# Optimization experiments

Hardware: AMD Instinct MI355X
Metric: run time of the kernel (lower is better)

## Reference

```python
import jax, jax.numpy as jnp
import numpy as np

DIM = 1024
HEADS = 16
HEAD_DIM = DIM // HEADS
EPS = 1e-5


def layer_norm(x, w, b):
    # normalize over last dim (head_dim)
    mu = jnp.mean(x, axis=-1, keepdims=True)
    var = jnp.mean(jnp.square(x - mu), axis=-1, keepdims=True)
    return (x - mu) * jax.lax.rsqrt(var + EPS) * w + b


def setup_inputs() -> dict:
    key = jax.random.key(0)
    ks = jax.random.split(key, 8)
    B, N = 2, 2048
    x = jax.random.normal(ks[0], (B, N, DIM), dtype=jnp.float32)
    mask = jax.random.randint(ks[1], (B, 1, N, N), 0, 2) == 1  # True = masked out
    qkv_w = jax.random.normal(ks[2], (3 * DIM, DIM), dtype=jnp.float32) * (DIM ** -0.5)
    q_norm_w = jnp.ones((HEAD_DIM,), dtype=jnp.float32)
    q_norm_b = jnp.zeros((HEAD_DIM,), dtype=jnp.float32)
    k_norm_w = jnp.ones((HEAD_DIM,), dtype=jnp.float32)
    k_norm_b = jnp.zeros((HEAD_DIM,), dtype=jnp.float32)
    proj_w = jax.random.normal(ks[3], (DIM, DIM), dtype=jnp.float32) * (DIM ** -0.5)
    proj_b = jnp.zeros((DIM,), dtype=jnp.float32)
    return {"x": x, "mask": mask, "qkv_w": qkv_w,
            "q_norm_w": q_norm_w, "q_norm_b": q_norm_b,
            "k_norm_w": k_norm_w, "k_norm_b": k_norm_b,
            "proj_w": proj_w, "proj_b": proj_b}


def reference(x, mask, qkv_w, q_norm_w, q_norm_b, k_norm_w, k_norm_b, proj_w, proj_b):
    B, N, C = x.shape
    H, D = HEADS, HEAD_DIM
    scale = D ** -0.5
    # qkv projection (no bias), split into q,k,v of shape (B,H,N,D)
    qkv = (x @ qkv_w.T).reshape(B, N, 3, H, D).transpose(2, 0, 3, 1, 4)
    q, k, v = qkv[0], qkv[1], qkv[2]
    q = layer_norm(q, q_norm_w, q_norm_b)
    k = layer_norm(k, k_norm_w, k_norm_b)
    q = q * scale
    attn = jnp.einsum("bhnd,bhmd->bhnm", q, k)  # (B,H,N,N)
    attn = jnp.where(mask, -jnp.inf, attn)
    attn = jax.nn.softmax(attn, axis=-1)
    out = jnp.einsum("bhnm,bhmd->bhnd", attn, v)
    out = out.transpose(0, 2, 1, 3).reshape(B, N, C)
    return out @ proj_w.T + proj_b
```

## Files before the change

kernel.cpp:

```cpp
#include <hip/hip_runtime.h>
#include <hip/hip_bf16.h>
#include <math.h>

#define B_    2
#define N_    2048
#define DIM_  1024
#define H_    16
#define HD_   64
#define EPS_  1e-5f
#define SCALE_ 0.125f
#define LOG2E_ 1.4426950408889634f
#define MFIX_  14.0f

typedef __attribute__((ext_vector_type(8))) __bf16 bf16x8;
typedef __attribute__((ext_vector_type(8))) unsigned short ushort8;
typedef __attribute__((ext_vector_type(4))) float f32x4;
typedef __attribute__((ext_vector_type(4))) unsigned int uint4v;

__device__ __forceinline__ unsigned short f2bf(float x) {
    unsigned u = __builtin_bit_cast(unsigned, x);
    u += 0x7fff + ((u >> 16) & 1);
    return (unsigned short)(u >> 16);
}
__device__ __forceinline__ unsigned pk2bf(float a, float b) {
    unsigned ua = __builtin_bit_cast(unsigned, a) + 0x8000u;
    unsigned ub = __builtin_bit_cast(unsigned, b) + 0x8000u;
    return __builtin_amdgcn_perm(ub, ua, 0x07060302);
}
__device__ __forceinline__ unsigned cvtpk(float a, float b) {
    unsigned r;
    asm("v_cvt_pk_bf16_f32 %0, %1, %2" : "=v"(r) : "v"(a), "v"(b));
    return r;
}

__device__ __forceinline__ void gl_lds16(const void* g, void* l) {
    __builtin_amdgcn_global_load_lds(
        (const __attribute__((address_space(1))) void*)g,
        (__attribute__((address_space(3))) void*)l, 16, 0, 0);
}

__global__ __launch_bounds__(256) void cast_all_bf16(
    const float* __restrict__ x, const float* __restrict__ qkvw,
    const float* __restrict__ pw, unsigned short* __restrict__ out) {
    int i = (blockIdx.x * 256 + threadIdx.x) * 8;
    const float* src;
    if (i < 4194304) src = x + i;
    else if (i < 7340032) src = qkvw + (i - 4194304);
    else src = pw + (i - 7340032);
    float4 v0 = *(const float4*)src;
    float4 v1 = *(const float4*)(src + 4);
    ushort8 r;
    r[0] = f2bf(v0.x); r[1] = f2bf(v0.y); r[2] = f2bf(v0.z); r[3] = f2bf(v0.w);
    r[4] = f2bf(v1.x); r[5] = f2bf(v1.y); r[6] = f2bf(v1.z); r[7] = f2bf(v1.w);
    *(ushort8*)(out + i) = r;
}

__global__ __launch_bounds__(256) void pack_mask(
    const int* __restrict__ mask, unsigned long long* __restrict__ bm) {
    int w = blockIdx.x * 4 + (threadIdx.x >> 6);
    int lane = threadIdx.x & 63;
    int mv = mask[(size_t)w * 64 + lane];
    unsigned long long bits = __ballot(mv != 0);
    if (lane == 0) bm[w] = bits;
}

__global__ __launch_bounds__(256) void gemm_qkv_ln(
    const unsigned short* __restrict__ A, const unsigned short* __restrict__ Bw,
    const float* __restrict__ qnw, const float* __restrict__ qnb,
    const float* __restrict__ knw, const float* __restrict__ knb,
    unsigned short* __restrict__ qbuf, unsigned short* __restrict__ kbuf,
    unsigned short* __restrict__ vt) {
    const int K = DIM_;
    __shared__ unsigned short As[128 * 32];
    __shared__ unsigned short Bs[128 * 32];
    const int tid = threadIdx.x;
    const int wave = tid >> 6, lane = tid & 63;
    const int quad = lane >> 4, lcol = lane & 15;
    const int wr = wave >> 1, wc = wave & 1;
    const int row0 = blockIdx.y * 128, col0 = blockIdx.x * 128;

    f32x4 acc[4][4];
#pragma unroll
    for (int i = 0; i < 4; ++i)
#pragma unroll
        for (int j = 0; j < 4; ++j) acc[i][j] = (f32x4){0.f, 0.f, 0.f, 0.f};

    for (int k0 = 0; k0 < K; k0 += 32) {
        __syncthreads();
#pragma unroll
        for (int c = 0; c < 2; ++c) {
            int base = wave * 2048 + c * 1024;
            int myofs = base + lane * 16;
            int r = myofs >> 6;
            int kb = myofs & 63;
            gl_lds16((const char*)A + ((size_t)(row0 + r) * K + k0) * 2 + kb,
                     (char*)As + base);
            gl_lds16((const char*)Bw + ((size_t)(col0 + r) * K + k0) * 2 + kb,
                     (char*)Bs + base);
        }
        __syncthreads();

        bf16x8 af[4], bfr[4];
#pragma unroll
        for (int i = 0; i < 4; ++i) {
            af[i] = *(const bf16x8*)&As[(wr * 64 + i * 16 + lcol) * 32 + quad * 8];
            bfr[i] = *(const bf16x8*)&Bs[(wc * 64 + i * 16 + lcol) * 32 + quad * 8];
        }
#pragma unroll
        for (int i = 0; i < 4; ++i)
#pragma unroll
            for (int j = 0; j < 4; ++j)
                acc[i][j] = __builtin_amdgcn_mfma_f32_16x16x32_bf16(
                    af[i], bfr[j], acc[i][j], 0, 0, 0);
    }

    const int colbase = col0 + wc * 64;
    const int t = colbase >> 10;
    const int h = (colbase & 1023) >> 6;

    if (t < 2) {
        const float* wv = (t == 0) ? qnw : knw;
        const float* bv = (t == 0) ? qnb : knb;
        float wreg[4], breg[4];
#pragma unroll
        for (int j = 0; j < 4; ++j) {
            wreg[j] = wv[j * 16 + lcol];
            breg[j] = bv[j * 16 + lcol];
        }
        const float sc = (t == 0) ? (SCALE_ * LOG2E_) : 1.f;
        unsigned short* obase = (t == 0) ? qbuf : kbuf;
#pragma unroll
        for (int i = 0; i < 4; ++i) {
#pragma unroll
            for (int reg = 0; reg < 4; ++reg) {
                int row = row0 + wr * 64 + i * 16 + quad * 4 + reg;
                int bb = row >> 11, n = row & (N_ - 1);
                float v[4];
#pragma unroll
                for (int j = 0; j < 4; ++j) v[j] = acc[i][j][reg];
                float s = v[0] + v[1] + v[2] + v[3];
                s += __shfl_xor(s, 1);
                s += __shfl_xor(s, 2);
                s += __shfl_xor(s, 4);
                s += __shfl_xor(s, 8);
                float mu = s * (1.f / 64.f);
                float d[4], s2 = 0.f;
#pragma unroll
                for (int j = 0; j < 4; ++j) {
                    d[j] = v[j] - mu;
                    s2 += d[j] * d[j];
                }
                s2 += __shfl_xor(s2, 1);
                s2 += __shfl_xor(s2, 2);
                s2 += __shfl_xor(s2, 4);
                s2 += __shfl_xor(s2, 8);
                float r = rsqrtf(s2 * (1.f / 64.f) + EPS_);
                float o0 = (d[0] * r * wreg[0] + breg[0]) * sc;
                float o1 = (d[1] * r * wreg[1] + breg[1]) * sc;
                float o2 = (d[2] * r * wreg[2] + breg[2]) * sc;
                float o3 = (d[3] * r * wreg[3] + breg[3]) * sc;
                uint2 pk;
                pk.x = pk2bf(o0, o1);
                pk.y = pk2bf(o2, o3);
                *(uint2*)(obase + ((size_t)(bb * H_ + h) * N_ + n) * 64 +
                          lcol * 4) = pk;
            }
        }
    } else {
        const int rowb = row0 + wr * 64;
        const int bb = rowb >> 11;
        unsigned short* vtb =
            vt + ((size_t)(bb * H_ + h) * 64) * (size_t)N_ + (rowb & (N_ - 1));
#pragma unroll
        for (int i = 0; i < 4; ++i) {
            const int pos = (i >> 1) * 32 + quad * 8 + (i & 1) * 4;
#pragma unroll
            for (int jj = 0; jj < 4; ++jj) {
                uint2 pk;
                pk.x = pk2bf(acc[i][jj][0], acc[i][jj][1]);
                pk.y = pk2bf(acc[i][jj][2], acc[i][jj][3]);
                *(uint2*)(vtb + (size_t)(lcol + 16 * jj) * N_ + pos) = pk;
            }
        }
    }
}

__global__ __launch_bounds__(256) void gemm_proj(
    const unsigned short* __restrict__ A, const unsigned short* __restrict__ Bw,
    const float* __restrict__ bias, float* __restrict__ Cout) {
    const int K = DIM_;
    __shared__ unsigned short As[128 * 32];
    __shared__ unsigned short Bs[64 * 32];
    const int tid = threadIdx.x;
    const int wave = tid >> 6, lane = tid & 63;
    const int quad = lane >> 4, lcol = lane & 15;
    const int row0 = blockIdx.y * 128, col0 = blockIdx.x * 64;

    f32x4 acc[2][4];
#pragma unroll
    for (int i = 0; i < 2; ++i)
#pragma unroll
        for (int j = 0; j < 4; ++j) acc[i][j] = (f32x4){0.f, 0.f, 0.f, 0.f};

    for (int k0 = 0; k0 < K; k0 += 32) {
        __syncthreads();
#pragma unroll
        for (int pi = 0; pi < 3; ++pi) {
            int p = wave * 3 + pi;
            if (p < 8) {
                int base = p * 1024;
                int myofs = base + lane * 16;
                int r = myofs >> 6, kb = myofs & 63;
                gl_lds16((const char*)A + ((size_t)(row0 + r) * K + k0) * 2 + kb,
                         (char*)As + base);
            } else {
                int base = (p - 8) * 1024;
                int myofs = base + lane * 16;
                int r = myofs >> 6, kb = myofs & 63;
                gl_lds16((const char*)Bw + ((size_t)(col0 + r) * K + k0) * 2 + kb,
                         (char*)Bs + base);
            }
        }
        __syncthreads();

        bf16x8 af[2], bfr[4];
#pragma unroll
        for (int i = 0; i < 2; ++i)
            af[i] = *(const bf16x8*)&As[(wave * 32 + i * 16 + lcol) * 32 + quad * 8];
#pragma unroll
        for (int j = 0; j < 4; ++j)
            bfr[j] = *(const bf16x8*)&Bs[(j * 16 + lcol) * 32 + quad * 8];
#pragma unroll
        for (int i = 0; i < 2; ++i)
#pragma unroll
            for (int j = 0; j < 4; ++j)
                acc[i][j] = __builtin_amdgcn_mfma_f32_16x16x32_bf16(
                    af[i], bfr[j], acc[i][j], 0, 0, 0);
    }

#pragma unroll
    for (int i = 0; i < 2; ++i) {
#pragma unroll
        for (int j = 0; j < 4; ++j) {
            int col = col0 + j * 16 + lcol;
            float bv = bias[col];
#pragma unroll
            for (int reg = 0; reg < 4; ++reg) {
                int row = row0 + wave * 32 + i * 16 + quad * 4 + reg;
                Cout[(size_t)row * DIM_ + col] = acc[i][j][reg] + bv;
            }
        }
    }
}

#define WB0                                                               \
    asm volatile("s_waitcnt vmcnt(0)" ::: "memory");                      \
    __builtin_amdgcn_s_barrier();                                         \
    __builtin_amdgcn_sched_barrier(0);

#define FISSUE(BUF, M0, M1)                                               \
    {                                                                     \
        gl_lds16(kp0, (char*)Ks[BUF] + kld0);                             \
        gl_lds16(kp1, (char*)Ks[BUF] + kld1);                             \
        gl_lds16(kp2, (char*)Ks[BUF] + kld2);                             \
        gl_lds16(kp3, (char*)Ks[BUF] + kld3);                             \
        gl_lds16(vp0, (char*)Vts[BUF] + kld0);                            \
        gl_lds16(vp1, (char*)Vts[BUF] + kld1);                            \
        gl_lds16(vp2, (char*)Vts[BUF] + kld2);                            \
        gl_lds16(vp3, (char*)Vts[BUF] + kld3);                            \
        M0 = *bmq0; M1 = *bmq1;                                           \
        kp0 += 8192; kp1 += 8192; kp2 += 8192; kp3 += 8192;               \
        vp0 += 128; vp1 += 128; vp2 += 128; vp3 += 128;                   \
        ++bmq0; ++bmq1;                                                   \
        __builtin_amdgcn_sched_barrier(0);                                \
    }

#define QKT(J, SACC, MWA, MWB)                                            \
    {                                                                     \
        unsigned long long mqa = (MWA) >> (quad * 4);                     \
        unsigned long long mqb = (MWB) >> (quad * 4);                     \
        unsigned ml[2][2];                                                \
        ml[0][0] = (unsigned)mqa; ml[0][1] = (unsigned)(mqa >> 32);       \
        ml[1][0] = (unsigned)mqb; ml[1][1] = (unsigned)(mqb >> 32);       \
        _Pragma("unroll")                                                 \
        for (int qf = 0; qf < 2; ++qf)                                    \
            _Pragma("unroll")                                             \
            for (int kt = 0; kt < 4; ++kt) {                              \
                unsigned word = ml[qf][kt >> 1];                          \
                _Pragma("unroll")                                         \
                for (int reg = 0; reg < 4; ++reg) {                       \
                    unsigned msk = (unsigned)(((int)(word <<              \
                        (31 - ((kt & 1) * 16 + reg)))) >> 31);            \
                    SACC[qf][kt][reg] = __builtin_bit_cast(float,         \
                        (msk & 0xc61c4000u) | (~msk & 0xc1600000u));      \
                }                                                         \
            }                                                             \
        __builtin_amdgcn_s_setprio(1);                                    \
        _Pragma("unroll")                                                 \
        for (int kt = 0; kt < 4; ++kt)                                    \
            _Pragma("unroll")                                             \
            for (int d0 = 0; d0 < 2; ++d0) {                              \
                bf16x8 ak = *(const bf16x8*)((const char*)Ks[J] +         \
                    (d0 * 4 + quad) * 1024 + kt * 256 + lofs);            \
                SACC[0][kt] = __builtin_amdgcn_mfma_f32_16x16x32_bf16(    \
                    ak, bq[0][d0], SACC[0][kt], 0, 0, 0);                 \
                SACC[1][kt] = __builtin_amdgcn_mfma_f32_16x16x32_bf16(    \
                    ak, bq[1][d0], SACC[1][kt], 0, 0, 0);                 \
            }                                                             \
        __builtin_amdgcn_s_setprio(0);                                    \
    }

#define SM(SACC, PK)                                                      \
    _Pragma("unroll")                                                     \
    for (int qf = 0; qf < 2; ++qf)                                        \
        _Pragma("unroll")                                                 \
        for (int kt = 0; kt < 4; ++kt) {                                  \
            float p0 = exp2f(SACC[qf][kt][0]);                            \
            float p1 = exp2f(SACC[qf][kt][1]);                            \
            float p2 = exp2f(SACC[qf][kt][2]);                            \
            float p3 = exp2f(SACC[qf][kt][3]);                            \
            PK[qf][kt].x = cvtpk(p0, p1);                                 \
            PK[qf][kt].y = cvtpk(p2, p3);                                 \
        }

#define PV(J, PK)                                                         \
    {                                                                     \
        __builtin_amdgcn_s_setprio(1);                                    \
        _Pragma("unroll")                                                 \
        for (int P = 0; P < 2; ++P) {                                     \
            bf16x8 bp[2];                                                 \
            _Pragma("unroll")                                             \
            for (int qf = 0; qf < 2; ++qf) {                              \
                uint4v bu;                                                \
                bu[0] = PK[qf][2 * P].x;  bu[1] = PK[qf][2 * P].y;        \
                bu[2] = PK[qf][2 * P + 1].x; bu[3] = PK[qf][2 * P + 1].y; \
                bp[qf] = __builtin_bit_cast(bf16x8, bu);                  \
                lacc[qf] = __builtin_amdgcn_mfma_f32_16x16x32_bf16(       \
                    ones, bp[qf], lacc[qf], 0, 0, 0);                     \
            }                                                             \
            _Pragma("unroll")                                             \
            for (int dt = 0; dt < 4; ++dt) {                              \
                bf16x8 va = *(const bf16x8*)((const char*)Vts[J] +        \
                    (P * 4 + quad) * 1024 + dt * 256 + lofs);             \
                oacc[0][dt] = __builtin_amdgcn_mfma_f32_16x16x32_bf16(    \
                    va, bp[0], oacc[0][dt], 0, 0, 0);                     \
                oacc[1][dt] = __builtin_amdgcn_mfma_f32_16x16x32_bf16(    \
                    va, bp[1], oacc[1][dt], 0, 0, 0);                     \
            }                                                             \
        }                                                                 \
        __builtin_amdgcn_s_setprio(0);                                    \
    }

#define TILE(J, M0, M1)                                                   \
    {                                                                     \
        f32x4 saccT[2][4];                                                \
        uint2 pkT[2][4];                                                  \
        QKT(J, saccT, M0, M1)                                             \
        SM(saccT, pkT)                                                    \
        PV(J, pkT)                                                        \
    }

__global__ __launch_bounds__(128, 2) void flash_attn_mfma10(
    const unsigned short* __restrict__ q, const unsigned short* __restrict__ k,
    const unsigned short* __restrict__ vt,
    const unsigned long long* __restrict__ bm, unsigned short* __restrict__ ao) {
    __shared__ unsigned short Qs[64 * 64];
    __shared__ unsigned short Ks[2][64 * 64];
    __shared__ unsigned short Vts[2][64 * 64];

    const int tid = threadIdx.x;
    const int wave = tid >> 6, lane = tid & 63;
    const int quad = lane >> 4, lcol = lane & 15;
    const int lid = blockIdx.y * 32 + blockIdx.x;
    const int bh = (lid & 7) * 4 + ((lid >> 3) & 3);
    const int q0 = (lid >> 5) * 64;
    const int b = bh >> 4, h = bh & 15;
    const int lofs = (lcol ^ (quad * 2)) << 4;

    const char* kgbase = (const char*)k + (size_t)bh * N_ * 128;
    const char* vtbase = (const char*)vt + (size_t)bh * 64 * N_ * 2;

    const int kld0 = (wave * 4 + 0) * 1024, kld1 = (wave * 4 + 1) * 1024;
    const int kld2 = (wave * 4 + 2) * 1024, kld3 = (wave * 4 + 3) * 1024;
    const char* kp0 = kgbase + (lane ^ 0) * 128 + (wave * 4 + 0) * 16;
    const char* kp1 = kgbase + (lane ^ 2) * 128 + (wave * 4 + 1) * 16;
    const char* kp2 = kgbase + (lane ^ 4) * 128 + (wave * 4 + 2) * 16;
    const char* kp3 = kgbase + (lane ^ 6) * 128 + (wave * 4 + 3) * 16;
    const char* vp0 = vtbase + (size_t)(lane ^ 0) * (N_ * 2) + (wave * 4 + 0) * 16;
    const char* vp1 = vtbase + (size_t)(lane ^ 2) * (N_ * 2) + (wave * 4 + 1) * 16;
    const char* vp2 = vtbase + (size_t)(lane ^ 4) * (N_ * 2) + (wave * 4 + 2) * 16;
    const char* vp3 = vtbase + (size_t)(lane ^ 6) * (N_ * 2) + (wave * 4 + 3) * 16;

    const unsigned long long* bmq0 =
        bm + ((size_t)b * N_ + q0 + wave * 32 + lcol) * 32;
    const unsigned long long* bmq1 = bmq0 + 16 * 32;
    unsigned long long mA0, mA1, mB0, mB1;

    {
        const char* qg = (const char*)(q + (size_t)(bh * N_ + q0) * 64);
#pragma unroll
        for (int c = 0; c < 4; ++c) {
            int base = wave * 4096 + c * 1024;
            gl_lds16(qg + base + lane * 16, (char*)Qs + base);
        }
    }
    asm volatile("" ::: "memory");
    __builtin_amdgcn_sched_barrier(0);
    FISSUE(0, mA0, mA1)
    asm volatile("s_waitcnt vmcnt(10)" ::: "memory");
    __builtin_amdgcn_sched_barrier(0);

    bf16x8 bq[2][2];
#pragma unroll
    for (int qf = 0; qf < 2; ++qf)
#pragma unroll
        for (int d0 = 0; d0 < 2; ++d0)
            bq[qf][d0] = *(const bf16x8*)&Qs[(wave * 32 + qf * 16 + lcol) * 64 +
                                             d0 * 32 + quad * 8];

    ushort8 ot;
#pragma unroll
    for (int i = 0; i < 8; ++i) ot[i] = 0x3F80;
    const bf16x8 ones = __builtin_bit_cast(bf16x8, ot);

    f32x4 oacc[2][4];
#pragma unroll
    for (int qf = 0; qf < 2; ++qf)
#pragma unroll
        for (int dt = 0; dt < 4; ++dt) oacc[qf][dt] = (f32x4){0.f, 0.f, 0.f, 0.f};
    f32x4 lacc[2];
    lacc[0] = (f32x4){0.f, 0.f, 0.f, 0.f};
    lacc[1] = (f32x4){0.f, 0.f, 0.f, 0.f};

    for (int g = 0; g < 15; ++g) {
        WB0 FISSUE(1, mB0, mB1) TILE(0, mA0, mA1)
        WB0 FISSUE(0, mA0, mA1) TILE(1, mB0, mB1)
    }
    WB0 FISSUE(1, mB0, mB1) TILE(0, mA0, mA1)
    WB0 TILE(1, mB0, mB1)

#pragma unroll
    for (int qf = 0; qf < 2; ++qf) {
        float inv = 1.f / lacc[qf][0];
        int row = q0 + wave * 32 + qf * 16 + lcol;
        unsigned short* dst =
            ao + ((size_t)(b * N_ + row)) * DIM_ + h * 64 + quad * 4;
#pragma unroll
        for (int dt = 0; dt < 4; ++dt) {
            uint2 pko;
            pko.x = pk2bf(oacc[qf][dt][0] * inv, oacc[qf][dt][1] * inv);
            pko.y = pk2bf(oacc[qf][dt][2] * inv, oacc[qf][dt][3] * inv);
            *(uint2*)(dst + dt * 16) = pko;
        }
    }
}

extern "C" void kernel_launch(void* const* d_in, const int* in_sizes, int n_in,
                              void* d_out, int out_size, void* d_ws,
                              size_t ws_size, hipStream_t stream) {
    const float* x     = (const float*)d_in[0];
    const int*   mask  = (const int*)d_in[1];
    const float* qkv_w = (const float*)d_in[2];
    const float* qnw   = (const float*)d_in[3];
    const float* qnb   = (const float*)d_in[4];
    const float* knw   = (const float*)d_in[5];
    const float* knb   = (const float*)d_in[6];
    const float* pw    = (const float*)d_in[7];
    const float* pb    = (const float*)d_in[8];
    float* out = (float*)d_out;

    char* ws = (char*)d_ws;
    unsigned short* x_bf  = (unsigned short*)(ws + 0);
    unsigned short* qw_bf = (unsigned short*)(ws + 8388608);
    unsigned short* pw_bf = (unsigned short*)(ws + 14680064);
    unsigned short* qbuf  = (unsigned short*)(ws + 16777216);
    unsigned short* kbuf  = (unsigned short*)(ws + 25165824);
    unsigned short* ao_bnc= (unsigned short*)(ws + 33554432);
    unsigned short* vt    = (unsigned short*)(ws + 41943040);
    unsigned long long* bmask = (unsigned long long*)(ws + 50331648);

    cast_all_bf16<<<8388608 / 2048, 256, 0, stream>>>(x, qkv_w, pw, x_bf);

    pack_mask<<<(B_ * N_ * (N_ / 64)) / 4, 256, 0, stream>>>(mask, bmask);

    gemm_qkv_ln<<<dim3(3072 / 128, 4096 / 128), 256, 0, stream>>>(
        x_bf, qw_bf, qnw, qnb, knw, knb, qbuf, kbuf, vt);

    flash_attn_mfma10<<<dim3(32, 32), 128, 0, stream>>>(
        qbuf, kbuf, vt, bmask, ao_bnc);

    gemm_proj<<<dim3(DIM_ / 64, 4096 / 128), 256, 0, stream>>>(
        ao_bnc, pw_bf, pb, out);
}
```

Baseline: 274.3 us.

## Split attention KV range across wave halves in larger blocks with LDS merge

The flash attention kernel moves from 128-thread blocks over 64 query rows to 512-thread blocks over 128 query rows. Each pair of waves handles 32 query rows, and each wave in the pair takes half of the key/value sequence with its own double-buffered K/V tiles. Each wave now issues half as many async global-to-LDS loads per tile, and the loop runs half as many iterations. The partial O and row sums from the second half are merged through shared memory before normalisation, which relies on the fixed max-offset softmax so no max rescaling is needed. This adds more parallelism per query block but uses about 80 KB of LDS per block and adds a cross-wave merge and an extra barrier.

```diff
diff --git a/kernel.cpp b/kernel.cpp
--- a/kernel.cpp
+++ b/kernel.cpp
@@ -260,22 +260,17 @@
 
 #define FISSUE(BUF, M0, M1)                                               \
     {                                                                     \
-        gl_lds16(kp0, (char*)Ks[BUF] + kld0);                             \
-        gl_lds16(kp1, (char*)Ks[BUF] + kld1);                             \
-        gl_lds16(kp2, (char*)Ks[BUF] + kld2);                             \
-        gl_lds16(kp3, (char*)Ks[BUF] + kld3);                             \
-        gl_lds16(vp0, (char*)Vts[BUF] + kld0);                            \
-        gl_lds16(vp1, (char*)Vts[BUF] + kld1);                            \
-        gl_lds16(vp2, (char*)Vts[BUF] + kld2);                            \
-        gl_lds16(vp3, (char*)Vts[BUF] + kld3);                            \
+        gl_lds16(kp0, ksb_base + (BUF) * 8192 + kld0);                    \
+        gl_lds16(kp1, ksb_base + (BUF) * 8192 + kld1);                    \
+        gl_lds16(vp0, vsb_base + (BUF) * 8192 + kld0);                    \
+        gl_lds16(vp1, vsb_base + (BUF) * 8192 + kld1);                    \
         M0 = *bmq0; M1 = *bmq1;                                           \
-        kp0 += 8192; kp1 += 8192; kp2 += 8192; kp3 += 8192;               \
-        vp0 += 128; vp1 += 128; vp2 += 128; vp3 += 128;                   \
+        kp0 += 8192; kp1 += 8192; vp0 += 128; vp1 += 128;                 \
         ++bmq0; ++bmq1;                                                   \
         __builtin_amdgcn_sched_barrier(0);                                \
     }
 
-#define QKT(J, SACC, MWA, MWB)                                            \
+#define QKT(KSB, SACC, MWA, MWB)                                          \
     {                                                                     \
         unsigned long long mqa = (MWA) >> (quad * 4);                     \
         unsigned long long mqb = (MWB) >> (quad * 4);                     \
@@ -300,7 +295,7 @@
         for (int kt = 0; kt < 4; ++kt)                                    \
             _Pragma("unroll")                                             \
             for (int d0 = 0; d0 < 2; ++d0) {                              \
-                bf16x8 ak = *(const bf16x8*)((const char*)Ks[J] +         \
+                bf16x8 ak = *(const bf16x8*)((KSB) +                      \
                     (d0 * 4 + quad) * 1024 + kt * 256 + lofs);            \
                 SACC[0][kt] = __builtin_amdgcn_mfma_f32_16x16x32_bf16(    \
                     ak, bq[0][d0], SACC[0][kt], 0, 0, 0);                 \
@@ -323,7 +318,7 @@
             PK[qf][kt].y = cvtpk(p2, p3);                                 \
         }
 
-#define PV(J, PK)                                                         \
+#define PV(VSB, PK)                                                       \
     {                                                                     \
         __builtin_amdgcn_s_setprio(1);                                    \
         _Pragma("unroll")                                                 \
@@ -340,7 +335,7 @@
             }                                                             \
             _Pragma("unroll")                                             \
             for (int dt = 0; dt < 4; ++dt) {                              \
-                bf16x8 va = *(const bf16x8*)((const char*)Vts[J] +        \
+                bf16x8 va = *(const bf16x8*)((VSB) +                      \
                     (P * 4 + quad) * 1024 + dt * 256 + lofs);             \
                 oacc[0][dt] = __builtin_amdgcn_mfma_f32_16x16x32_bf16(    \
                     va, bp[0], oacc[0][dt], 0, 0, 0);                     \
@@ -355,67 +350,68 @@
     {                                                                     \
         f32x4 saccT[2][4];                                                \
         uint2 pkT[2][4];                                                  \
-        QKT(J, saccT, M0, M1)                                             \
+        QKT(ksb_base + (J) * 8192, saccT, M0, M1)                         \
         SM(saccT, pkT)                                                    \
-        PV(J, pkT)                                                        \
-    }
-
-__global__ __launch_bounds__(128, 2) void flash_attn_mfma10(
+        PV(vsb_base + (J) * 8192, pkT)                                    \
+    }
+
+__global__ __launch_bounds__(512, 4) void flash_attn_mfma12(
     const unsigned short* __restrict__ q, const unsigned short* __restrict__ k,
     const unsigned short* __restrict__ vt,
     const unsigned long long* __restrict__ bm, unsigned short* __restrict__ ao) {
-    __shared__ unsigned short Qs[64 * 64];
-    __shared__ unsigned short Ks[2][64 * 64];
-    __shared__ unsigned short Vts[2][64 * 64];
+    __shared__ __align__(16) char smem[81920];
+    unsigned short* Qs = (unsigned short*)smem;
 
     const int tid = threadIdx.x;
     const int wave = tid >> 6, lane = tid & 63;
     const int quad = lane >> 4, lcol = lane & 15;
-    const int lid = blockIdx.y * 32 + blockIdx.x;
-    const int bh = (lid & 7) * 4 + ((lid >> 3) & 3);
-    const int q0 = (lid >> 5) * 64;
-    const int b = bh >> 4, h = bh & 15;
+    const int p = wave >> 1;
+    const int hf = wave & 1;
+    const int bh = blockIdx.y, b = bh >> 4, h = bh & 15;
+    const int q0 = blockIdx.x * 128;
     const int lofs = (lcol ^ (quad * 2)) << 4;
+
+    char* const ksb_base = smem + 16384 + hf * 16384;
+    char* const vsb_base = smem + 49152 + hf * 16384;
 
     const char* kgbase = (const char*)k + (size_t)bh * N_ * 128;
     const char* vtbase = (const char*)vt + (size_t)bh * 64 * N_ * 2;
 
-    const int kld0 = (wave * 4 + 0) * 1024, kld1 = (wave * 4 + 1) * 1024;
-    const int kld2 = (wave * 4 + 2) * 1024, kld3 = (wave * 4 + 3) * 1024;
-    const char* kp0 = kgbase + (lane ^ 0) * 128 + (wave * 4 + 0) * 16;
-    const char* kp1 = kgbase + (lane ^ 2) * 128 + (wave * 4 + 1) * 16;
-    const char* kp2 = kgbase + (lane ^ 4) * 128 + (wave * 4 + 2) * 16;
-    const char* kp3 = kgbase + (lane ^ 6) * 128 + (wave * 4 + 3) * 16;
-    const char* vp0 = vtbase + (size_t)(lane ^ 0) * (N_ * 2) + (wave * 4 + 0) * 16;
-    const char* vp1 = vtbase + (size_t)(lane ^ 2) * (N_ * 2) + (wave * 4 + 1) * 16;
-    const char* vp2 = vtbase + (size_t)(lane ^ 4) * (N_ * 2) + (wave * 4 + 2) * 16;
-    const char* vp3 = vtbase + (size_t)(lane ^ 6) * (N_ * 2) + (wave * 4 + 3) * 16;
+    const int c0 = p * 2, c1 = p * 2 + 1;
+    const int swz0 = (c0 & 3) * 2, swz1 = (c1 & 3) * 2;
+    const int kld0 = c0 * 1024, kld1 = c1 * 1024;
+    const char* kp0 = kgbase + ((size_t)hf << 17) + (lane ^ swz0) * 128 + c0 * 16;
+    const char* kp1 = kgbase + ((size_t)hf << 17) + (lane ^ swz1) * 128 + c1 * 16;
+    const char* vp0 = vtbase + hf * 2048 + (size_t)(lane ^ swz0) * (N_ * 2) + c0 * 16;
+    const char* vp1 = vtbase + hf * 2048 + (size_t)(lane ^ swz1) * (N_ * 2) + c1 * 16;
 
     const unsigned long long* bmq0 =
-        bm + ((size_t)b * N_ + q0 + wave * 32 + lcol) * 32;
+        bm + ((size_t)b * N_ + q0 + p * 32 + lcol) * 32 + hf * 16;
     const unsigned long long* bmq1 = bmq0 + 16 * 32;
     unsigned long long mA0, mA1, mB0, mB1;
 
     {
         const char* qg = (const char*)(q + (size_t)(bh * N_ + q0) * 64);
 #pragma unroll
-        for (int c = 0; c < 4; ++c) {
-            int base = wave * 4096 + c * 1024;
+        for (int c = 0; c < 2; ++c) {
+            int base = wave * 2048 + c * 1024;
             gl_lds16(qg + base + lane * 16, (char*)Qs + base);
         }
     }
     asm volatile("" ::: "memory");
     __builtin_amdgcn_sched_barrier(0);
     FISSUE(0, mA0, mA1)
-    asm volatile("s_waitcnt vmcnt(10)" ::: "memory");
+    asm volatile("s_waitcnt vmcnt(6)" ::: "memory");
     __builtin_amdgcn_sched_barrier(0);
+    __builtin_amdgcn_s_barrier();
+    __builtin_amdgcn_sched_barrier(0);
 
     bf16x8 bq[2][2];
 #pragma unroll
     for (int qf = 0; qf < 2; ++qf)
 #pragma unroll
         for (int d0 = 0; d0 < 2; ++d0)
-            bq[qf][d0] = *(const bf16x8*)&Qs[(wave * 32 + qf * 16 + lcol) * 64 +
+            bq[qf][d0] = *(const bf16x8*)&Qs[(p * 32 + qf * 16 + lcol) * 64 +
                                              d0 * 32 + quad * 8];
 
     ushort8 ot;
@@ -432,25 +428,45 @@
     lacc[0] = (f32x4){0.f, 0.f, 0.f, 0.f};
     lacc[1] = (f32x4){0.f, 0.f, 0.f, 0.f};
 
-    for (int g = 0; g < 15; ++g) {
+    for (int g = 0; g < 7; ++g) {
         WB0 FISSUE(1, mB0, mB1) TILE(0, mA0, mA1)
         WB0 FISSUE(0, mA0, mA1) TILE(1, mB0, mB1)
     }
     WB0 FISSUE(1, mB0, mB1) TILE(0, mA0, mA1)
     WB0 TILE(1, mB0, mB1)
 
-#pragma unroll
-    for (int qf = 0; qf < 2; ++qf) {
-        float inv = 1.f / lacc[qf][0];
-        int row = q0 + wave * 32 + qf * 16 + lcol;
-        unsigned short* dst =
-            ao + ((size_t)(b * N_ + row)) * DIM_ + h * 64 + quad * 4;
-#pragma unroll
-        for (int dt = 0; dt < 4; ++dt) {
-            uint2 pko;
-            pko.x = pk2bf(oacc[qf][dt][0] * inv, oacc[qf][dt][1] * inv);
-            pko.y = pk2bf(oacc[qf][dt][2] * inv, oacc[qf][dt][3] * inv);
-            *(uint2*)(dst + dt * 16) = pko;
+    __syncthreads();
+    float* mb = (float*)(smem + 16384);
+    if (hf) {
+        float* dst = mb + (p * 64 + lane) * 41;
+#pragma unroll
+        for (int qf = 0; qf < 2; ++qf)
+#pragma unroll
+            for (int dt = 0; dt < 4; ++dt)
+#pragma unroll
+                for (int r = 0; r < 4; ++r)
+                    dst[qf * 16 + dt * 4 + r] = oacc[qf][dt][r];
+        dst[32] = lacc[0][0];
+        dst[33] = lacc[1][0];
+    }
+    __syncthreads();
+    if (!hf) {
+        const float* src = mb + (p * 64 + lane) * 41;
+#pragma unroll
+        for (int qf = 0; qf < 2; ++qf) {
+            float inv = 1.f / (lacc[qf][0] + src[32 + qf]);
+            int row = q0 + p * 32 + qf * 16 + lcol;
+            unsigned short* dst2 =
+                ao + ((size_t)(b * N_ + row)) * DIM_ + h * 64 + quad * 4;
+#pragma unroll
+            for (int dt = 0; dt < 4; ++dt) {
+                uint2 pko;
+                pko.x = pk2bf((oacc[qf][dt][0] + src[qf * 16 + dt * 4 + 0]) * inv,
+                              (oacc[qf][dt][1] + src[qf * 16 + dt * 4 + 1]) * inv);
+                pko.y = pk2bf((oacc[qf][dt][2] + src[qf * 16 + dt * 4 + 2]) * inv,
+                              (oacc[qf][dt][3] + src[qf * 16 + dt * 4 + 3]) * inv);
+                *(uint2*)(dst2 + dt * 16) = pko;
+            }
         }
     }
 }
@@ -486,7 +502,7 @@
     gemm_qkv_ln<<<dim3(3072 / 128, 4096 / 128), 256, 0, stream>>>(
         x_bf, qw_bf, qnw, qnb, knw, knb, qbuf, kbuf, vt);
 
-    flash_attn_mfma10<<<dim3(32, 32), 128, 0, stream>>>(
+    flash_attn_mfma12<<<dim3(N_ / 128, B_ * H_), 512, 0, stream>>>(
         qbuf, kbuf, vt, bmask, ao_bnc);
 
     gemm_proj<<<dim3(DIM_ / 64, 4096 / 128), 256, 0, stream>>>(
```

New measurement: 289.3 us. 5.5% more time.
